# Optimization experiments

Hardware: AMD Instinct MI355X
Metric: run time of the kernel (lower is better)

The kernel has to match this reference:

```python
import jax, jax.numpy as jnp
import numpy as np

DIM = 1024
HEADS = 16
HIDDEN = 2048  # dim * mlp_ratio
EPS = 1e-6


def _rmsnorm(x, scale):
    # faithful to torch: x * (scale / (norm / (sqrt(d) + eps)))
    norm = jnp.linalg.norm(x, axis=-1, keepdims=True)
    return x * (scale * (x.shape[-1] ** 0.5 + EPS) / norm)


def setup_inputs() -> dict:
    key = jax.random.key(0)
    ks = jax.random.split(key, 8)
    B, N, C = 4, 4096, DIM
    s = 0.02
    return {
        "x": jax.random.normal(ks[0], (B, N, C), dtype=jnp.float32),
        "scale1": jnp.ones((C,), jnp.float32),
        "scale2": jnp.ones((C,), jnp.float32),
        "gamma": jnp.ones((C,), jnp.float32),
        "qkv_w": jax.random.normal(ks[1], (3 * C, C), jnp.float32) * s,
        "proj_w": jax.random.normal(ks[2], (C, C), jnp.float32) * s,
        "proj_b": jnp.zeros((C,), jnp.float32),
        "conv1_w": jax.random.normal(ks[3], (HIDDEN, C), jnp.float32) * s,
        "conv1_b": jnp.zeros((HIDDEN,), jnp.float32),
        "conv2_w": jax.random.normal(ks[4], (C, HIDDEN), jnp.float32) * s,
        "conv2_b": jnp.zeros((C,), jnp.float32),
    }


def reference(x, scale1, scale2, gamma, qkv_w, proj_w, proj_b,
              conv1_w, conv1_b, conv2_w, conv2_b):
    B, N, C = x.shape
    h, d = HEADS, C // HEADS

    # ---- attention branch ----
    xn = _rmsnorm(x, scale1)
    qkv = jnp.einsum('bnc,fc->bnf', xn, qkv_w)           # [B,N,3C]
    qkv = qkv.reshape(B, N, 3, h, d).transpose(2, 0, 3, 1, 4)  # [3,B,h,N,d]
    q, k, v = qkv[0], qkv[1], qkv[2]
    phi = lambda t: jnp.exp(-0.5 * t * t)
    q, k = phi(q), phi(k)
    kv = jnp.einsum('bhnd,bhne->bhde', k, v)             # [B,h,d,d]
    z = 1.0 / (jnp.einsum('bhnd,bhd->bhn', q, k.sum(2)) + 1e-6)
    out = jnp.einsum('bhnd,bhde,bhn->bhne', q, kv, z)    # [B,h,N,d]
    out = out.transpose(0, 2, 1, 3).reshape(B, N, C)
    attn = jnp.einsum('bnc,oc->bno', out, proj_w) + proj_b
    x = x + gamma * attn

    # ---- MLP branch (1x1 convs == per-token linear) ----
    xn2 = _rmsnorm(x, scale2)
    hdd = jax.nn.gelu(jnp.einsum('bnc,hc->bnh', xn2, conv1_w) + conv1_b, approximate=False)
    mlp = jnp.einsum('bnh,ch->bnc', hdd, conv2_w) + conv2_b
    return x + gamma * mlp
```

## Files before the change

### kernel.cpp

```cpp
#include <hip/hip_runtime.h>
#include <hip/hip_bf16.h>
#include <math.h>

#define MTOK 16384

typedef __attribute__((ext_vector_type(8))) short bf16x8;
typedef __attribute__((ext_vector_type(4))) float f32x4;

__device__ __forceinline__ float bf2f(ushort u) {
  union { unsigned int u; float f; } c; c.u = ((unsigned int)u) << 16; return c.f;
}
__device__ __forceinline__ ushort f2bf(float f) {
  __hip_bfloat16 h = __float2bfloat16(f);
  return *(ushort*)&h;
}

__device__ __forceinline__ void gload_lds16(const void* g, void* l) {
  __builtin_amdgcn_global_load_lds(
      (const __attribute__((address_space(1))) unsigned int*)g,
      (__attribute__((address_space(3))) unsigned int*)l, 16, 0, 0);
}

__global__ __launch_bounds__(256)
void prep_k(const float* __restrict__ qkv_w, ushort* __restrict__ wq,
            const float* __restrict__ proj_w, ushort* __restrict__ wp,
            const float* __restrict__ conv1_w, ushort* __restrict__ w1,
            const float* __restrict__ conv2_w, ushort* __restrict__ w2,
            const float* __restrict__ gamma,
            const float* __restrict__ proj_b, const float* __restrict__ conv2_b,
            float* __restrict__ gbp, float* __restrict__ gbc,
            float* __restrict__ zero1, float* __restrict__ sumsq,
            const float* __restrict__ x, const float* __restrict__ scale1,
            ushort* __restrict__ xn) {
  int b = blockIdx.x, t = threadIdx.x;
  if (b < 3072) {
    int i = b * 256 + t;
    float4 v = *(const float4*)&qkv_w[(size_t)i * 4];
    ushort4 o = {f2bf(v.x), f2bf(v.y), f2bf(v.z), f2bf(v.w)};
    *(ushort4*)&wq[(size_t)i * 4] = o;
  } else if (b < 4096) {
    int i = (b - 3072) * 256 + t;
    float g = gamma[(i * 4) >> 10];
    float4 v = *(const float4*)&proj_w[(size_t)i * 4];
    ushort4 o = {f2bf(v.x * g), f2bf(v.y * g), f2bf(v.z * g), f2bf(v.w * g)};
    *(ushort4*)&wp[(size_t)i * 4] = o;
  } else if (b < 6144) {
    int i = (b - 4096) * 256 + t;
    float4 v = *(const float4*)&conv1_w[(size_t)i * 4];
    ushort4 o = {f2bf(v.x), f2bf(v.y), f2bf(v.z), f2bf(v.w)};
    *(ushort4*)&w1[(size_t)i * 4] = o;
  } else if (b < 8192) {
    int i = (b - 6144) * 256 + t;
    float g = gamma[(i * 4) >> 11];
    float4 v = *(const float4*)&conv2_w[(size_t)i * 4];
    ushort4 o = {f2bf(v.x * g), f2bf(v.y * g), f2bf(v.z * g), f2bf(v.w * g)};
    *(ushort4*)&w2[(size_t)i * 4] = o;
  } else if (b < 8200) {
    int i = (b - 8192) * 256 + t;
    if (i < 1024) gbp[i] = gamma[i] * proj_b[i];
    else if (i < 2048) gbc[i - 1024] = gamma[i - 1024] * conv2_b[i - 1024];
  } else if (b < 8460) {
    int i = (b - 8200) * 256 + t;
    if (i < 66560) ((float4*)zero1)[i] = (float4){0.f, 0.f, 0.f, 0.f};
  } else if (b < 8476) {
    int i = (b - 8460) * 256 + t;
    if (i < 4096) ((float4*)sumsq)[i] = (float4){0.f, 0.f, 0.f, 0.f};
  } else {
    __shared__ float red[4];
    int row = b - 8476;
    const float* xr = x + (size_t)row * 1024;
    float4 v = *(const float4*)&xr[t * 4];
    float s = v.x*v.x + v.y*v.y + v.z*v.z + v.w*v.w;
    #pragma unroll
    for (int off = 32; off > 0; off >>= 1) s += __shfl_xor(s, off);
    if ((t & 63) == 0) red[t >> 6] = s;
    __syncthreads();
    float tot = red[0] + red[1] + red[2] + red[3];
    float rn = (32.0f + 1e-6f) / sqrtf(tot);
    float4 sc = *(const float4*)&scale1[t * 4];
    ushort4 o;
    o.x = f2bf(v.x * rn * sc.x);
    o.y = f2bf(v.y * rn * sc.y);
    o.z = f2bf(v.z * rn * sc.z);
    o.w = f2bf(v.w * rn * sc.w);
    *(ushort4*)&xn[(size_t)row * 1024 + t * 4] = o;
  }
}

template<int EPI>
__global__ __launch_bounds__(512, 6)
void gemm_bt(const ushort* __restrict__ A, const ushort* __restrict__ W,
             void* __restrict__ outp, const float* __restrict__ bias,
             const float* __restrict__ resid,
             ushort* __restrict__ kTp, ushort* __restrict__ vTp,
             const float* __restrict__ escale, const float* __restrict__ sumsq_in,
             float* __restrict__ sumsq, ushort* __restrict__ xnout,
             int M, int F, int K) {
  __shared__ ushort lA[2][128 * 32];
  __shared__ ushort lB[2][128 * 32];
  const int tid = threadIdx.x;
  const int lane = tid & 63;
  const int w = tid >> 6;
  const int wm = w >> 2, wn = w & 3;
  const int nBn = F >> 7;
  const int cpx = (int)gridDim.x >> 3;
  const int tile = ((int)blockIdx.x & 7) * cpx + ((int)blockIdx.x >> 3);
  const int bm = tile / nBn;
  const int bn = tile % nBn;
  const int brow = bm << 7, bcol = bn << 7;

  const int srow = (w << 4) + (lane >> 2);
  const int key = (srow >> 1) & 3;
  const int kcsrc = (lane & 3) ^ key;
  const ushort* gA0 = A + (size_t)(brow + srow) * K + kcsrc * 8;
  const ushort* gB0 = W + (size_t)(bcol + srow) * K + kcsrc * 8;

  auto stage = [&](int bf, int k0) {
    gload_lds16(gA0 + k0, &lA[bf][w * 512]);
    gload_lds16(gB0 + k0, &lB[bf][w * 512]);
  };

  const int frow = lane & 15;
  const int kq = lane >> 4;

  f32x4 acc[4][2];
  #pragma unroll
  for (int i = 0; i < 4; ++i)
    #pragma unroll
    for (int j = 0; j < 2; ++j) acc[i][j] = (f32x4){0.f, 0.f, 0.f, 0.f};

  stage(0, 0);
  __syncthreads();

  int buf = 0;
  for (int k0 = 0; k0 < K; k0 += 32, buf ^= 1) {
    if (k0 + 32 < K) stage(buf ^ 1, k0 + 32);

    bf16x8 af[4], bfr[2];
    #pragma unroll
    for (int mi = 0; mi < 4; ++mi) {
      int row = (wm << 6) + (mi << 4) + frow;
      int off = (row << 5) + ((kq ^ ((row >> 1) & 3)) << 3);
      af[mi] = *(const bf16x8*)&lA[buf][off];
    }
    #pragma unroll
    for (int ni = 0; ni < 2; ++ni) {
      int row = (wn << 5) + (ni << 4) + frow;
      int off = (row << 5) + ((kq ^ ((row >> 1) & 3)) << 3);
      bfr[ni] = *(const bf16x8*)&lB[buf][off];
    }
    #pragma unroll
    for (int mi = 0; mi < 4; ++mi)
      #pragma unroll
      for (int ni = 0; ni < 2; ++ni)
        acc[mi][ni] = __builtin_amdgcn_mfma_f32_16x16x32_bf16(
            af[mi], bfr[ni], acc[mi][ni], 0, 0, 0);
    __syncthreads();
  }

  #pragma unroll
  for (int mi = 0; mi < 4; ++mi) {
    const int rbase = brow + (wm << 6) + (mi << 4) + (kq << 2);
    float ss[4] = {0.f, 0.f, 0.f, 0.f};
    float rsc[4];
    if (EPI == 2) {
      #pragma unroll
      for (int r = 0; r < 4; ++r)
        rsc[r] = (32.0f + 1e-6f) * __frsqrt_rn(sumsq_in[rbase + r]);
    }
    #pragma unroll
    for (int ni = 0; ni < 2; ++ni) {
      int col = bcol + (wn << 5) + (ni << 4) + frow;
      if (EPI == 0) {
        if (col < 1024) {
          #pragma unroll
          for (int r = 0; r < 4; ++r) {
            float v = acc[mi][ni][r];
            ((ushort*)outp)[(size_t)(rbase + r) * 1024 + col] =
                f2bf(__expf(-0.5f * v * v));
          }
        } else {
          bool isk = col < 2048;
          int c = col - (isk ? 1024 : 2048);
          int b = rbase >> 12, n = rbase & 4095;
          ushort4 o;
          #pragma unroll
          for (int r = 0; r < 4; ++r) {
            float v = acc[mi][ni][r];
            if (isk) v = __expf(-0.5f * v * v);
            ((ushort*)&o)[r] = f2bf(v);
          }
          ushort* dst = (isk ? kTp : vTp) +
                        ((size_t)(b * 16 + (c >> 6)) * 64 + (c & 63)) * 4096 + n;
          *(ushort4*)dst = o;
        }
      } else if (EPI == 1) {
        #pragma unroll
        for (int r = 0; r < 4; ++r) {
          size_t idx = (size_t)(rbase + r) * F + col;
          ((float*)outp)[idx] = resid[idx] + acc[mi][ni][r] + bias[col];
        }
      } else if (EPI == 2) {
        #pragma unroll
        for (int r = 0; r < 4; ++r) {
          float t2 = acc[mi][ni][r] * rsc[r] + bias[col];
          float y = 0.79788456f * (t2 + 0.044715f * t2 * t2 * t2);
          float e = __expf(2.0f * y);
          float th = (e - 1.0f) / (e + 1.0f);
          ((ushort*)outp)[(size_t)(rbase + r) * F + col] =
              f2bf(0.5f * t2 * (1.0f + th));
        }
      } else {
        #pragma unroll
        for (int r = 0; r < 4; ++r) {
          size_t idx = (size_t)(rbase + r) * F + col;
          float x1 = resid[idx] + acc[mi][ni][r] + bias[col];
          ((float*)outp)[idx] = x1;
          xnout[idx] = f2bf(x1 * escale[col]);
          ss[r] += x1 * x1;
        }
      }
    }
    if (EPI == 3) {
      #pragma unroll
      for (int r = 0; r < 4; ++r) {
        #pragma unroll
        for (int m = 1; m < 16; m <<= 1) ss[r] += __shfl_xor(ss[r], m);
      }
      if (frow == 0) {
        #pragma unroll
        for (int r = 0; r < 4; ++r) atomicAdd(&sumsq[rbase + r], ss[r]);
      }
    }
  }
}

__global__ __launch_bounds__(256)
void attn_kv_mfma(const ushort* __restrict__ kT, const ushort* __restrict__ vT,
                  float* __restrict__ kvT, float* __restrict__ ksum) {
  __shared__ float red[4][4096];
  int bi = blockIdx.x;
  int ksl = bi & 7, h = (bi >> 3) & 15, b = bi >> 7;
  int tid = threadIdx.x, lane = tid & 63, w = tid >> 6;
  int frow = lane & 15, kq = lane >> 4;
  const size_t bh = (size_t)(b * 16 + h) * 64;
  const ushort* vb = vT + bh * 4096;
  const ushort* kb = kT + bh * 4096;
  int tk0 = ksl * 512 + w * 128;

  f32x4 acc[4][4];
  #pragma unroll
  for (int i = 0; i < 4; ++i)
    #pragma unroll
    for (int j = 0; j < 4; ++j) acc[i][j] = (f32x4){0.f, 0.f, 0.f, 0.f};
  float kpart[4] = {0.f, 0.f, 0.f, 0.f};

  #pragma unroll
  for (int kstep = 0; kstep < 4; ++kstep) {
    int tok = tk0 + kstep * 32 + kq * 8;
    bf16x8 af[4], bfr[4];
    #pragma unroll
    for (int mi = 0; mi < 4; ++mi)
      af[mi] = *(const bf16x8*)&vb[(size_t)(mi * 16 + frow) * 4096 + tok];
    #pragma unroll
    for (int ni = 0; ni < 4; ++ni) {
      bfr[ni] = *(const bf16x8*)&kb[(size_t)(ni * 16 + frow) * 4096 + tok];
      #pragma unroll
      for (int j = 0; j < 8; ++j) kpart[ni] += bf2f((ushort)bfr[ni][j]);
    }
    #pragma unroll
    for (int mi = 0; mi < 4; ++mi)
      #pragma unroll
      for (int ni = 0; ni < 4; ++ni)
        acc[mi][ni] = __builtin_amdgcn_mfma_f32_16x16x32_bf16(
            af[mi], bfr[ni], acc[mi][ni], 0, 0, 0);
  }

  #pragma unroll
  for (int ni = 0; ni < 4; ++ni) {
    kpart[ni] += __shfl_xor(kpart[ni], 16);
    kpart[ni] += __shfl_xor(kpart[ni], 32);
  }
  if (lane < 16) {
    #pragma unroll
    for (int ni = 0; ni < 4; ++ni)
      atomicAdd(&ksum[(b * 16 + h) * 64 + ni * 16 + frow], kpart[ni]);
  }

  #pragma unroll
  for (int mi = 0; mi < 4; ++mi)
    #pragma unroll
    for (int ni = 0; ni < 4; ++ni)
      #pragma unroll
      for (int r = 0; r < 4; ++r)
        red[w][(mi * 16 + kq * 4 + r) * 64 + ni * 16 + frow] = acc[mi][ni][r];
  __syncthreads();
  float* kvg = kvT + (size_t)(b * 16 + h) * 4096;
  for (int i = tid; i < 4096; i += 256) {
    float s = red[0][i] + red[1][i] + red[2][i] + red[3][i];
    atomicAdd(&kvg[i], s);
  }
}

__global__ __launch_bounds__(256)
void attn_out_mfma(const ushort* __restrict__ qb, const float* __restrict__ kvT,
                   const float* __restrict__ ksum, ushort* __restrict__ ao) {
  __shared__ ushort skv[64 * 72];
  __shared__ float sks[64];
  int bi = blockIdx.x;
  int c = bi & 15, h = (bi >> 4) & 15, b = bi >> 8;
  int tid = threadIdx.x, lane = tid & 63, w = tid >> 6;
  int frow = lane & 15, kq = lane >> 4;
  const float* kvg = kvT + (size_t)(b * 16 + h) * 4096;
  for (int i = tid; i < 4096; i += 256)
    skv[(i >> 6) * 72 + (i & 63)] = f2bf(kvg[i]);
  if (tid < 64) sks[tid] = ksum[(b * 16 + h) * 64 + tid];
  __syncthreads();

  int m0 = b * 4096 + c * 256 + w * 64;
  f32x4 acc[4][4];
  #pragma unroll
  for (int i = 0; i < 4; ++i)
    #pragma unroll
    for (int j = 0; j < 4; ++j) acc[i][j] = (f32x4){0.f, 0.f, 0.f, 0.f};
  float dp[4] = {0.f, 0.f, 0.f, 0.f};

  #pragma unroll
  for (int kst = 0; kst < 2; ++kst) {
    int d0 = kst * 32 + kq * 8;
    bf16x8 af[4], bfr[4];
    #pragma unroll
    for (int mi = 0; mi < 4; ++mi)
      af[mi] = *(const bf16x8*)&qb[(size_t)(m0 + mi * 16 + frow) * 1024 + h * 64 + d0];
    #pragma unroll
    for (int ni = 0; ni < 4; ++ni)
      bfr[ni] = *(const bf16x8*)&skv[(ni * 16 + frow) * 72 + d0];
    #pragma unroll
    for (int mi = 0; mi < 4; ++mi) {
      float s = 0.f;
      #pragma unroll
      for (int j = 0; j < 8; ++j) s += bf2f((ushort)af[mi][j]) * sks[d0 + j];
      dp[mi] += s;
    }
    #pragma unroll
    for (int mi = 0; mi < 4; ++mi)
      #pragma unroll
      for (int ni = 0; ni < 4; ++ni)
        acc[mi][ni] = __builtin_amdgcn_mfma_f32_16x16x32_bf16(
            af[mi], bfr[ni], acc[mi][ni], 0, 0, 0);
  }

  #pragma unroll
  for (int mi = 0; mi < 4; ++mi) {
    dp[mi] += __shfl_xor(dp[mi], 16);
    dp[mi] += __shfl_xor(dp[mi], 32);
  }

  #pragma unroll
  for (int mi = 0; mi < 4; ++mi)
    #pragma unroll
    for (int ni = 0; ni < 4; ++ni)
      #pragma unroll
      for (int r = 0; r < 4; ++r) {
        float dotv = __shfl(dp[mi], (kq << 2) + r);
        float z = 1.f / (dotv + 1e-6f);
        int mrow = m0 + mi * 16 + kq * 4 + r;
        ao[(size_t)mrow * 1024 + h * 64 + ni * 16 + frow] =
            f2bf(acc[mi][ni][r] * z);
      }
}

extern "C" void kernel_launch(void* const* d_in, const int* in_sizes, int n_in,
                              void* d_out, int out_size, void* d_ws, size_t ws_size,
                              hipStream_t stream) {
  const float* x       = (const float*)d_in[0];
  const float* scale1  = (const float*)d_in[1];
  const float* scale2  = (const float*)d_in[2];
  const float* gamma   = (const float*)d_in[3];
  const float* qkv_w   = (const float*)d_in[4];
  const float* proj_w  = (const float*)d_in[5];
  const float* proj_b  = (const float*)d_in[6];
  const float* conv1_w = (const float*)d_in[7];
  const float* conv1_b = (const float*)d_in[8];
  const float* conv2_w = (const float*)d_in[9];
  const float* conv2_b = (const float*)d_in[10];
  float* out = (float*)d_out;

  char* ws = (char*)d_ws;
  size_t off = 0;
  auto alloc = [&](size_t bytes) {
    void* p = ws + off;
    off += (bytes + 255) & ~(size_t)255;
    return p;
  };
  ushort* xn     = (ushort*)alloc((size_t)MTOK * 1024 * 2);
  ushort* qb     = (ushort*)alloc((size_t)MTOK * 1024 * 2);
  ushort* kT     = (ushort*)alloc((size_t)MTOK * 1024 * 2);
  ushort* vT     = (ushort*)alloc((size_t)MTOK * 1024 * 2);
  ushort* attn_o = (ushort*)alloc((size_t)MTOK * 1024 * 2);
  float*  kvT    = (float*)alloc((size_t)(4 * 16 * 64 * 64 + 4 * 16 * 64) * 4);
  float*  ksum   = kvT + 4 * 16 * 64 * 64;
  ushort* wq = (ushort*)alloc((size_t)3072 * 1024 * 2);
  ushort* wp = (ushort*)alloc((size_t)1024 * 1024 * 2);
  ushort* w1 = (ushort*)alloc((size_t)2048 * 1024 * 2);
  ushort* w2 = (ushort*)alloc((size_t)1024 * 2048 * 2);
  float*  gbp = (float*)alloc(1024 * 4);
  float*  gbc = (float*)alloc(1024 * 4);
  float*  sumsq = (float*)alloc(MTOK * 4);
  ushort* hid = kT;
  if (off > ws_size) return;

  prep_k<<<8476 + MTOK, 256, 0, stream>>>(qkv_w, wq, proj_w, wp, conv1_w, w1,
                                          conv2_w, w2, gamma, proj_b, conv2_b,
                                          gbp, gbc, kvT, sumsq, x, scale1, xn);

  gemm_bt<0><<<128 * 24, 512, 0, stream>>>(xn, wq, qb, nullptr, nullptr,
                                           kT, vT, nullptr, nullptr, nullptr, nullptr,
                                           MTOK, 3072, 1024);
  attn_kv_mfma<<<512, 256, 0, stream>>>(kT, vT, kvT, ksum);
  attn_out_mfma<<<1024, 256, 0, stream>>>(qb, kvT, ksum, attn_o);
  gemm_bt<3><<<128 * 8, 512, 0, stream>>>(attn_o, wp, out, gbp, x,
                                          nullptr, nullptr, scale2, nullptr,
                                          sumsq, xn, MTOK, 1024, 1024);

  gemm_bt<2><<<128 * 16, 512, 0, stream>>>(xn, w1, hid, conv1_b, nullptr,
                                           nullptr, nullptr, nullptr, sumsq,
                                           nullptr, nullptr, MTOK, 2048, 1024);
  gemm_bt<1><<<128 * 8, 512, 0, stream>>>(hid, w2, out, gbc, out,
                                          nullptr, nullptr, nullptr, nullptr,
                                          nullptr, nullptr, MTOK, 1024, 2048);
}
```

Baseline: 470.9 us.

## Load GEMM weight fragments directly from global and halve threads per block

```diff
diff --git a/kernel.cpp b/kernel.cpp
--- a/kernel.cpp
+++ b/kernel.cpp
@@ -88,7 +88,7 @@
 }
 
 template<int EPI>
-__global__ __launch_bounds__(512, 6)
+__global__ __launch_bounds__(256, 2)
 void gemm_bt(const ushort* __restrict__ A, const ushort* __restrict__ W,
              void* __restrict__ outp, const float* __restrict__ bias,
              const float* __restrict__ resid,
@@ -97,62 +97,65 @@
              float* __restrict__ sumsq, ushort* __restrict__ xnout,
              int M, int F, int K) {
   __shared__ ushort lA[2][128 * 32];
-  __shared__ ushort lB[2][128 * 32];
   const int tid = threadIdx.x;
   const int lane = tid & 63;
   const int w = tid >> 6;
-  const int wm = w >> 2, wn = w & 3;
   const int nBn = F >> 7;
   const int cpx = (int)gridDim.x >> 3;
   const int tile = ((int)blockIdx.x & 7) * cpx + ((int)blockIdx.x >> 3);
   const int bm = tile / nBn;
   const int bn = tile % nBn;
   const int brow = bm << 7, bcol = bn << 7;
+  const int wr = w >> 1, wc = w & 1;
 
   const int srow = (w << 4) + (lane >> 2);
   const int key = (srow >> 1) & 3;
   const int kcsrc = (lane & 3) ^ key;
   const ushort* gA0 = A + (size_t)(brow + srow) * K + kcsrc * 8;
-  const ushort* gB0 = W + (size_t)(bcol + srow) * K + kcsrc * 8;
-
-  auto stage = [&](int bf, int k0) {
+  const ushort* gA1 = gA0 + (size_t)64 * K;
+
+  auto stageA = [&](int bf, int k0) {
     gload_lds16(gA0 + k0, &lA[bf][w * 512]);
-    gload_lds16(gB0 + k0, &lB[bf][w * 512]);
+    gload_lds16(gA1 + k0, &lA[bf][2048 + w * 512]);
   };
 
   const int frow = lane & 15;
   const int kq = lane >> 4;
 
-  f32x4 acc[4][2];
+  const ushort* gB[4];
+  #pragma unroll
+  for (int ni = 0; ni < 4; ++ni)
+    gB[ni] = W + (size_t)(bcol + (wc << 6) + (ni << 4) + frow) * K + (kq << 3);
+
+  f32x4 acc[4][4];
   #pragma unroll
   for (int i = 0; i < 4; ++i)
     #pragma unroll
-    for (int j = 0; j < 2; ++j) acc[i][j] = (f32x4){0.f, 0.f, 0.f, 0.f};
-
-  stage(0, 0);
+    for (int j = 0; j < 4; ++j) acc[i][j] = (f32x4){0.f, 0.f, 0.f, 0.f};
+
+  stageA(0, 0);
   __syncthreads();
 
   int buf = 0;
   for (int k0 = 0; k0 < K; k0 += 32, buf ^= 1) {
-    if (k0 + 32 < K) stage(buf ^ 1, k0 + 32);
-
-    bf16x8 af[4], bfr[2];
+    bf16x8 bfr[4];
+    #pragma unroll
+    for (int ni = 0; ni < 4; ++ni)
+      bfr[ni] = *(const bf16x8*)(gB[ni] + k0);
+
+    if (k0 + 32 < K) stageA(buf ^ 1, k0 + 32);
+
+    bf16x8 af[4];
     #pragma unroll
     for (int mi = 0; mi < 4; ++mi) {
-      int row = (wm << 6) + (mi << 4) + frow;
+      int row = (wr << 6) + (mi << 4) + frow;
       int off = (row << 5) + ((kq ^ ((row >> 1) & 3)) << 3);
       af[mi] = *(const bf16x8*)&lA[buf][off];
     }
     #pragma unroll
-    for (int ni = 0; ni < 2; ++ni) {
-      int row = (wn << 5) + (ni << 4) + frow;
-      int off = (row << 5) + ((kq ^ ((row >> 1) & 3)) << 3);
-      bfr[ni] = *(const bf16x8*)&lB[buf][off];
-    }
-    #pragma unroll
     for (int mi = 0; mi < 4; ++mi)
       #pragma unroll
-      for (int ni = 0; ni < 2; ++ni)
+      for (int ni = 0; ni < 4; ++ni)
         acc[mi][ni] = __builtin_amdgcn_mfma_f32_16x16x32_bf16(
             af[mi], bfr[ni], acc[mi][ni], 0, 0, 0);
     __syncthreads();
@@ -160,7 +163,7 @@
 
   #pragma unroll
   for (int mi = 0; mi < 4; ++mi) {
-    const int rbase = brow + (wm << 6) + (mi << 4) + (kq << 2);
+    const int rbase = brow + (wr << 6) + (mi << 4) + (kq << 2);
     float ss[4] = {0.f, 0.f, 0.f, 0.f};
     float rsc[4];
     if (EPI == 2) {
@@ -169,8 +172,8 @@
         rsc[r] = (32.0f + 1e-6f) * __frsqrt_rn(sumsq_in[rbase + r]);
     }
     #pragma unroll
-    for (int ni = 0; ni < 2; ++ni) {
-      int col = bcol + (wn << 5) + (ni << 4) + frow;
+    for (int ni = 0; ni < 4; ++ni) {
+      int col = bcol + (wc << 6) + (ni << 4) + frow;
       if (EPI == 0) {
         if (col < 1024) {
           #pragma unroll
@@ -414,19 +417,19 @@
                                           conv2_w, w2, gamma, proj_b, conv2_b,
                                           gbp, gbc, kvT, sumsq, x, scale1, xn);
 
-  gemm_bt<0><<<128 * 24, 512, 0, stream>>>(xn, wq, qb, nullptr, nullptr,
+  gemm_bt<0><<<128 * 24, 256, 0, stream>>>(xn, wq, qb, nullptr, nullptr,
                                            kT, vT, nullptr, nullptr, nullptr, nullptr,
                                            MTOK, 3072, 1024);
   attn_kv_mfma<<<512, 256, 0, stream>>>(kT, vT, kvT, ksum);
   attn_out_mfma<<<1024, 256, 0, stream>>>(qb, kvT, ksum, attn_o);
-  gemm_bt<3><<<128 * 8, 512, 0, stream>>>(attn_o, wp, out, gbp, x,
+  gemm_bt<3><<<128 * 8, 256, 0, stream>>>(attn_o, wp, out, gbp, x,
                                           nullptr, nullptr, scale2, nullptr,
                                           sumsq, xn, MTOK, 1024, 1024);
 
-  gemm_bt<2><<<128 * 16, 512, 0, stream>>>(xn, w1, hid, conv1_b, nullptr,
+  gemm_bt<2><<<128 * 16, 256, 0, stream>>>(xn, w1, hid, conv1_b, nullptr,
                                            nullptr, nullptr, nullptr, sumsq,
                                            nullptr, nullptr, MTOK, 2048, 1024);
-  gemm_bt<1><<<128 * 8, 512, 0, stream>>>(hid, w2, out, gbc, out,
+  gemm_bt<1><<<128 * 8, 256, 0, stream>>>(hid, w2, out, gbc, out,
                                           nullptr, nullptr, nullptr, nullptr,
                                           nullptr, nullptr, MTOK, 1024, 2048);
 }
```

Result: slower. 691.9 us (+46.9%).
